# Kernel tuning notes

Measured on AMD Instinct MI355X. Metric: run time of the kernel, lower is better.

## Reference

```python
import jax, jax.numpy as jnp
import numpy as np

N_CODES = 1024
CODE_DIM = 256
B, T = 64, 1024


def setup_inputs() -> dict:
    key = jax.random.key(0)
    k1, k2 = jax.random.split(key)
    inputs = jax.random.normal(k1, (B, CODE_DIM, T), dtype=jnp.float32)
    embed = jax.random.normal(k2, (N_CODES, CODE_DIM), dtype=jnp.float32)
    return {"inputs": inputs, "embed": embed, "training": 0}


def reference(inputs, embed, training):
    # inputs: [B, D, T] -> [B, T, D]
    x = jnp.transpose(inputs, (0, 2, 1))
    Bsz, Tlen, D = x.shape
    flat = x.reshape(-1, D)  # [N, D], N = B*T
    distances = (
        jnp.sum(flat * flat, axis=1, keepdims=True)
        - 2.0 * jnp.matmul(flat, embed.T)
        + jnp.sum(embed * embed, axis=1)
    )  # [N, n_codes]
    encoding_indices = jnp.argmin(distances, axis=1)  # [N]
    # gather instead of one-hot matmul (same math)
    quantized = embed[encoding_indices].reshape(x.shape)  # [B, T, D]

    sg = jax.lax.stop_gradient
    codebook_loss = jnp.mean((sg(quantized) - x) ** 2)
    cmt_loss = jnp.mean((quantized - sg(x)) ** 2)
    loss = codebook_loss + cmt_loss * 0.2

    # straight-through estimator
    quantized_st = x + sg(quantized - x)
    quantized_out = jnp.transpose(quantized_st, (0, 2, 1))  # [B, D, T]

    # avg one-hot probabilities via bincount-style scatter-add
    n = flat.shape[0]
    counts = jnp.zeros((N_CODES,), dtype=flat.dtype).at[encoding_indices].add(1.0)
    avg_probs = counts / n
    perplexity = jnp.exp(-jnp.sum(avg_probs * jnp.log(avg_probs + 1e-10)))

    encoding_indices_out = encoding_indices.reshape(Bsz, -1, 1)
    return (quantized_out, loss, cmt_loss, encoding_indices_out, perplexity)
```

## Files before the change

### kernel.cpp

```cpp
#include <hip/hip_runtime.h>

#define B_ 64
#define D_ 256
#define T_ 1024
#define NC_ 1024
#define DT_ (D_ * T_)
#define NPTS_ (B_ * T_)

#define QSZ_   16777216
#define LOSS_OFF 16777216
#define CMT_OFF  16777217
#define IDX_OFF  16777218
#define PERP_OFF 16842754

typedef _Float16 half8 __attribute__((ext_vector_type(8)));
typedef float f32x4 __attribute__((ext_vector_type(4)));

#define XROW_ 264
#define XLO_OFF_ (64 * XROW_)

__global__ void prep_embed(const float* __restrict__ embed,
                           _Float16* __restrict__ ehi,
                           _Float16* __restrict__ elo,
                           float* __restrict__ normf) {
  int g = blockIdx.x;
  int tid = threadIdx.x;
  int w = tid >> 6, l = tid & 63;

#pragma unroll
  for (int ii = 0; ii < 2; ++ii) {
    int kc = w * 2 + ii;
    int code = g * 16 + (l & 15);
    int k0 = kc * 32 + (l >> 4) * 8;
    const float* src = embed + (size_t)code * D_ + k0;
    half8 hh, ll;
#pragma unroll
    for (int j = 0; j < 8; ++j) {
      float v = src[j];
      _Float16 h = (_Float16)v;
      _Float16 lo = (_Float16)(v - (float)h);
      hh[j] = h;
      ll[j] = lo;
    }
    size_t off = ((size_t)(g * 8 + kc) * 64 + l) * 8;
    *(half8*)(ehi + off) = hh;
    *(half8*)(elo + off) = ll;
  }

  int code = g * 16 + (tid >> 4);
  int ks = (tid & 15) * 16;
  const float* src = embed + (size_t)code * D_ + ks;
  double s = 0.0;
#pragma unroll
  for (int j = 0; j < 16; ++j) {
    double v = src[j];
    s += v * v;
  }
#pragma unroll
  for (int m = 1; m < 16; m <<= 1) s += __shfl_xor(s, m, 64);
  if ((tid & 15) == 0) normf[code] = (float)s;
}

__global__ __launch_bounds__(256, 2) void argmin_kernel(
    const float* __restrict__ inputs, const _Float16* __restrict__ ehi,
    const _Float16* __restrict__ elo, const float* __restrict__ normf,
    float* __restrict__ idx_out, int* __restrict__ counts,
    double* __restrict__ mse_acc) {
  __shared__ _Float16 xs[2 * 64 * XROW_];
  __shared__ float normf_lds[1024];
  __shared__ double part[256];
  __shared__ double xn2s[64];

  float* candv = (float*)part;
  int* candi = (int*)&part[128];

  int tid = threadIdx.x;
  int blk = blockIdx.x;
  int b = blk >> 4, t0 = (blk & 15) * 64;
  size_t base = (size_t)b * DT_ + t0;

  {
    int t = tid & 63, dgrp = tid >> 6;
    const float* src = inputs + base + t;
    double s = 0.0;
#pragma unroll 4
    for (int i = 0; i < 32; ++i) {
      int d = dgrp * 64 + i * 2;
      float v0 = src[(size_t)d * T_];
      float v1 = src[(size_t)(d + 1) * T_];
      s += (double)v0 * v0 + (double)v1 * v1;
      _Float16 h0 = (_Float16)v0, h1 = (_Float16)v1;
      _Float16 e0 = (_Float16)(v0 - (float)h0);
      _Float16 e1 = (_Float16)(v1 - (float)h1);
      union {
        _Float16 h[2];
        unsigned u;
      } ph, pl;
      ph.h[0] = h0; ph.h[1] = h1;
      pl.h[0] = e0; pl.h[1] = e1;
      *(unsigned*)&xs[t * XROW_ + d] = ph.u;
      *(unsigned*)&xs[XLO_OFF_ + t * XROW_ + d] = pl.u;
    }
    part[tid] = s;
    ((float4*)normf_lds)[tid] = ((const float4*)normf)[tid];
  }
  __syncthreads();
  if (tid < 64)
    xn2s[tid] = part[tid] + part[64 + tid] + part[128 + tid] + part[192 + tid];
  __syncthreads();

  int w = tid >> 6, l = tid & 63;
  int lrow = l & 15;
  int lk = (l >> 4) * 8;

  float bestv[4][4];
  int besti[4][4];
#pragma unroll
  for (int m = 0; m < 4; ++m)
#pragma unroll
    for (int r = 0; r < 4; ++r) {
      bestv[m][r] = 1e30f;
      besti[m][r] = 0;
    }

#pragma unroll 1
  for (int ng = 0; ng < 4; ++ng) {
    f32x4 acc[4][4];
#pragma unroll
    for (int m = 0; m < 4; ++m)
#pragma unroll
      for (int n = 0; n < 4; ++n) acc[m][n] = (f32x4){0.f, 0.f, 0.f, 0.f};

#pragma unroll 2
    for (int kc = 0; kc < 8; ++kc) {
      half8 bh[4], bl[4];
#pragma unroll
      for (int n = 0; n < 4; ++n) {
        int g = ng * 16 + w * 4 + n;
        size_t off = ((size_t)(g * 8 + kc) * 64 + l) * 8;
        bh[n] = *(const half8*)(ehi + off);
        bl[n] = *(const half8*)(elo + off);
      }
      half8 ah[4], al[4];
#pragma unroll
      for (int m = 0; m < 4; ++m) {
        const _Float16* p = &xs[(m * 16 + lrow) * XROW_ + kc * 32 + lk];
        ah[m] = *(const half8*)p;
        al[m] = *(const half8*)(p + XLO_OFF_);
      }
#pragma unroll
      for (int m = 0; m < 4; ++m)
#pragma unroll
        for (int n = 0; n < 4; ++n) {
          acc[m][n] =
              __builtin_amdgcn_mfma_f32_16x16x32_f16(ah[m], bh[n], acc[m][n], 0, 0, 0);
          acc[m][n] =
              __builtin_amdgcn_mfma_f32_16x16x32_f16(al[m], bh[n], acc[m][n], 0, 0, 0);
          acc[m][n] =
              __builtin_amdgcn_mfma_f32_16x16x32_f16(ah[m], bl[n], acc[m][n], 0, 0, 0);
        }
    }

#pragma unroll
    for (int n = 0; n < 4; ++n) {
      int c = ng * 256 + w * 64 + n * 16 + lrow;
      float nf = normf_lds[c];
#pragma unroll
      for (int m = 0; m < 4; ++m)
#pragma unroll
        for (int r = 0; r < 4; ++r) {
          float df = fmaf(-2.0f, acc[m][n][r], nf);
          if (df < bestv[m][r]) {
            bestv[m][r] = df;
            besti[m][r] = c;
          }
        }
    }
  }

#pragma unroll
  for (int msk = 1; msk < 16; msk <<= 1) {
#pragma unroll
    for (int m = 0; m < 4; ++m)
#pragma unroll
      for (int r = 0; r < 4; ++r) {
        float ov = __shfl_xor(bestv[m][r], msk, 64);
        int oi = __shfl_xor(besti[m][r], msk, 64);
        if (ov < bestv[m][r] || (ov == bestv[m][r] && oi < besti[m][r])) {
          bestv[m][r] = ov;
          besti[m][r] = oi;
        }
      }
  }
  if (lrow == 0) {
    int q = l >> 4;
#pragma unroll
    for (int m = 0; m < 4; ++m)
#pragma unroll
      for (int r = 0; r < 4; ++r) {
        candv[w * 64 + m * 16 + q * 4 + r] = bestv[m][r];
        candi[w * 64 + m * 16 + q * 4 + r] = besti[m][r];
      }
  }
  __syncthreads();

  if (tid < 64) {
    float bv = candv[tid];
    int bi = candi[tid];
#pragma unroll
    for (int w2 = 1; w2 < 4; ++w2) {
      float ov = candv[w2 * 64 + tid];
      int oi = candi[w2 * 64 + tid];
      if (ov < bv || (ov == bv && oi < bi)) {
        bv = ov;
        bi = oi;
      }
    }
    int p = blk * 64 + tid;
    idx_out[p] = (float)bi;
    atomicAdd(&counts[bi], 1);
    double s = xn2s[tid] + (double)bv;
    for (int msk = 32; msk; msk >>= 1) s += __shfl_down(s, msk, 64);
    if (tid == 0) atomicAdd(mse_acc, s);
  }
}

__global__ __launch_bounds__(256) void quantize_kernel(
    const float* __restrict__ embed, const float* __restrict__ idx_f,
    float* __restrict__ qout) {
  __shared__ float qs[64 * 257];
  __shared__ int lidx[64];

  int tid = threadIdx.x;
  int bx = blockIdx.x;
  int b = bx >> 4;
  int t0 = (bx & 15) * 64;

  if (tid < 64) lidx[tid] = (int)idx_f[b * T_ + t0 + tid];
  __syncthreads();

#pragma unroll 4
  for (int p = 0; p < 64; ++p) {
    qs[p * 257 + tid] = embed[(size_t)lidx[p] * D_ + tid];
  }
  __syncthreads();

  size_t base = (size_t)b * DT_ + t0;
#pragma unroll 4
  for (int i = 0; i < 64; ++i) {
    int d = i * 4 + (tid >> 6);
    int p = tid & 63;
    qout[base + (size_t)d * T_ + p] = qs[p * 257 + d];
  }
}

__global__ void finalize_kernel(const int* __restrict__ counts,
                                const double* __restrict__ mse_acc,
                                float* __restrict__ out) {
  int tid = threadIdx.x;
  double p = (double)counts[tid] / (double)NPTS_;
  double s = p * log(p + 1e-10);
  for (int m = 32; m; m >>= 1) s += __shfl_down(s, m, 64);
  __shared__ double red[16];
  if ((tid & 63) == 0) red[tid >> 6] = s;
  __syncthreads();
  if (tid == 0) {
    double tot = 0.0;
    for (int i = 0; i < 16; ++i) tot += red[i];
    double mse = *mse_acc / (double)QSZ_;
    out[LOSS_OFF] = (float)(mse * 1.2);
    out[CMT_OFF] = (float)mse;
    out[PERP_OFF] = (float)exp(-tot);
  }
}

extern "C" void kernel_launch(void* const* d_in, const int* in_sizes, int n_in,
                              void* d_out, int out_size, void* d_ws,
                              size_t ws_size, hipStream_t stream) {
  const float* inputs = (const float*)d_in[0];
  const float* embed = (const float*)d_in[1];
  float* out = (float*)d_out;

  char* ws = (char*)d_ws;
  _Float16* ehi = (_Float16*)ws;
  _Float16* elo = (_Float16*)(ws + 524288);
  float* normf = (float*)(ws + 1048576);
  int* counts = (int*)(ws + 1048576 + 4096);
  double* mse = (double*)(ws + 1048576 + 8192);

  hipMemsetAsync(ws + 1048576 + 4096, 0, 4096 + 8, stream);

  prep_embed<<<64, 256, 0, stream>>>(embed, ehi, elo, normf);
  argmin_kernel<<<1024, 256, 0, stream>>>(inputs, ehi, elo, normf,
                                          out + IDX_OFF, counts, mse);
  quantize_kernel<<<1024, 256, 0, stream>>>(embed, out + IDX_OFF, out);
  finalize_kernel<<<1, 1024, 0, stream>>>(counts, mse, out);
}
```

Baseline: 151.2 us.

## Software-pipeline argmin MFMA loop with double-buffered operands and narrower code tiles

Restructures the argmin GEMM loop so each wave handles 2 code tiles per group across 8 groups instead of 4 tiles across 4 groups. Loads for the next k-chunk of global B and LDS A fragments are issued into a second register buffer while MFMAs run on the current one. The aim is to hide global and LDS latency behind matrix math and cut accumulator register pressure. In exchange, the X fragments are now reloaded from LDS twice as often, and the last step prefetches group 0 again, which is wasted work.

Measured after the change: 339.4 us. 124% more time.

```diff
diff --git a/kernel.cpp b/kernel.cpp
--- a/kernel.cpp
+++ b/kernel.cpp
@@ -59,6 +59,46 @@
 #pragma unroll
   for (int m = 1; m < 16; m <<= 1) s += __shfl_xor(s, m, 64);
   if ((tid & 15) == 0) normf[code] = (float)s;
+}
+
+__device__ __forceinline__ void loadB2(half8 (&BH)[2], half8 (&BL)[2],
+                                       const _Float16* __restrict__ ehi,
+                                       const _Float16* __restrict__ elo,
+                                       int w, int l, int ng, int kc) {
+#pragma unroll
+  for (int n = 0; n < 2; ++n) {
+    int g = ng * 8 + w * 2 + n;
+    size_t off = ((size_t)(g * 8 + kc) * 64 + l) * 8;
+    BH[n] = *(const half8*)(ehi + off);
+    BL[n] = *(const half8*)(elo + off);
+  }
+}
+
+__device__ __forceinline__ void loadA(half8 (&AH)[4], half8 (&AL)[4],
+                                      const _Float16* xs, int lrow, int lk,
+                                      int kc) {
+#pragma unroll
+  for (int m = 0; m < 4; ++m) {
+    const _Float16* p = &xs[(m * 16 + lrow) * XROW_ + kc * 32 + lk];
+    AH[m] = *(const half8*)p;
+    AL[m] = *(const half8*)(p + XLO_OFF_);
+  }
+}
+
+__device__ __forceinline__ void mfma24(f32x4 (&acc)[4][2], half8 (&AH)[4],
+                                       half8 (&AL)[4], half8 (&BH)[2],
+                                       half8 (&BL)[2]) {
+#pragma unroll
+  for (int m = 0; m < 4; ++m)
+#pragma unroll
+    for (int n = 0; n < 2; ++n) {
+      acc[m][n] =
+          __builtin_amdgcn_mfma_f32_16x16x32_f16(AH[m], BH[n], acc[m][n], 0, 0, 0);
+      acc[m][n] =
+          __builtin_amdgcn_mfma_f32_16x16x32_f16(AL[m], BH[n], acc[m][n], 0, 0, 0);
+      acc[m][n] =
+          __builtin_amdgcn_mfma_f32_16x16x32_f16(AH[m], BL[n], acc[m][n], 0, 0, 0);
+    }
 }
 
 __global__ __launch_bounds__(256, 2) void argmin_kernel(
@@ -72,7 +112,7 @@
   __shared__ double xn2s[64];
 
   float* candv = (float*)part;
-  int* candi = (int*)&part[128];
+  int* candi = (int*)(part + 128);
 
   int tid = threadIdx.x;
   int blk = blockIdx.x;
@@ -123,47 +163,42 @@
       besti[m][r] = 0;
     }
 
+  half8 ahA[4], alA[4], ahB[4], alB[4];
+  half8 bhA[2], blA[2], bhB[2], blB[2];
+  loadB2(bhA, blA, ehi, elo, w, l, 0, 0);
+  loadA(ahA, alA, xs, lrow, lk, 0);
+
+#define STEP_TO_B(NGB, KCB, KCA)                       \
+  loadB2(bhB, blB, ehi, elo, w, l, NGB, KCB);          \
+  loadA(ahB, alB, xs, lrow, lk, KCA);                  \
+  mfma24(acc, ahA, alA, bhA, blA);
+
+#define STEP_TO_A(NGB, KCB, KCA)                       \
+  loadB2(bhA, blA, ehi, elo, w, l, NGB, KCB);          \
+  loadA(ahA, alA, xs, lrow, lk, KCA);                  \
+  mfma24(acc, ahB, alB, bhB, blB);
+
 #pragma unroll 1
-  for (int ng = 0; ng < 4; ++ng) {
-    f32x4 acc[4][4];
+  for (int ng = 0; ng < 8; ++ng) {
+    f32x4 acc[4][2];
 #pragma unroll
     for (int m = 0; m < 4; ++m)
 #pragma unroll
-      for (int n = 0; n < 4; ++n) acc[m][n] = (f32x4){0.f, 0.f, 0.f, 0.f};
-
-#pragma unroll 2
-    for (int kc = 0; kc < 8; ++kc) {
-      half8 bh[4], bl[4];
-#pragma unroll
-      for (int n = 0; n < 4; ++n) {
-        int g = ng * 16 + w * 4 + n;
-        size_t off = ((size_t)(g * 8 + kc) * 64 + l) * 8;
-        bh[n] = *(const half8*)(ehi + off);
-        bl[n] = *(const half8*)(elo + off);
-      }
-      half8 ah[4], al[4];
-#pragma unroll
-      for (int m = 0; m < 4; ++m) {
-        const _Float16* p = &xs[(m * 16 + lrow) * XROW_ + kc * 32 + lk];
-        ah[m] = *(const half8*)p;
-        al[m] = *(const half8*)(p + XLO_OFF_);
-      }
-#pragma unroll
-      for (int m = 0; m < 4; ++m)
-#pragma unroll
-        for (int n = 0; n < 4; ++n) {
-          acc[m][n] =
-              __builtin_amdgcn_mfma_f32_16x16x32_f16(ah[m], bh[n], acc[m][n], 0, 0, 0);
-          acc[m][n] =
-              __builtin_amdgcn_mfma_f32_16x16x32_f16(al[m], bh[n], acc[m][n], 0, 0, 0);
-          acc[m][n] =
-              __builtin_amdgcn_mfma_f32_16x16x32_f16(ah[m], bl[n], acc[m][n], 0, 0, 0);
-        }
-    }
-
-#pragma unroll
-    for (int n = 0; n < 4; ++n) {
-      int c = ng * 256 + w * 64 + n * 16 + lrow;
+      for (int n = 0; n < 2; ++n) acc[m][n] = (f32x4){0.f, 0.f, 0.f, 0.f};
+
+    int ngn = (ng + 1) & 7;
+    STEP_TO_B(ng, 1, 1)
+    STEP_TO_A(ng, 2, 2)
+    STEP_TO_B(ng, 3, 3)
+    STEP_TO_A(ng, 4, 4)
+    STEP_TO_B(ng, 5, 5)
+    STEP_TO_A(ng, 6, 6)
+    STEP_TO_B(ng, 7, 7)
+    STEP_TO_A(ngn, 0, 0)
+
+#pragma unroll
+    for (int n = 0; n < 2; ++n) {
+      int c = (ng * 8 + w * 2 + n) * 16 + lrow;
       float nf = normf_lds[c];
 #pragma unroll
       for (int m = 0; m < 4; ++m)
@@ -177,6 +212,8 @@
         }
     }
   }
+#undef STEP_TO_B
+#undef STEP_TO_A
 
 #pragma unroll
   for (int msk = 1; msk < 16; msk <<= 1) {
```

## Keep input tile in registers and stream codebook through double-buffered LDS

Applied to the files above, without the earlier changes.

Each wave now holds its own 16 points' split-f16 A fragments in registers for the whole K range. The hi/lo codebook is streamed in 16-code chunks into double-buffered LDS using global_load_lds, so all four waves share each chunk instead of each wave reading its own codes from global memory. This removes the per-wave global B traffic and the cross-wave argmin reduction, and raises occupancy to 3 blocks per CU. In exchange it needs a barrier every one of 64 iterations and does only one MFMA chain per iteration, which may leave latency exposed. It also relies on every lane of a predicated group reaching the atomics and shuffles correctly.

Result: slower. 176.8 us (+16.9%).

```diff
diff --git a/kernel.cpp b/kernel.cpp
--- a/kernel.cpp
+++ b/kernel.cpp
@@ -16,9 +16,6 @@
 typedef _Float16 half8 __attribute__((ext_vector_type(8)));
 typedef float f32x4 __attribute__((ext_vector_type(4)));
 
-#define XROW_ 264
-#define XLO_OFF_ (64 * XROW_)
-
 __global__ void prep_embed(const float* __restrict__ embed,
                            _Float16* __restrict__ ehi,
                            _Float16* __restrict__ elo,
@@ -61,167 +58,135 @@
   if ((tid & 15) == 0) normf[code] = (float)s;
 }
 
-__global__ __launch_bounds__(256, 2) void argmin_kernel(
+__device__ __forceinline__ void gld_lds16(const _Float16* gsrc_lane,
+                                          _Float16* lds_base) {
+  __builtin_amdgcn_global_load_lds(
+      (const __attribute__((address_space(1))) void*)gsrc_lane,
+      (__attribute__((address_space(3))) void*)lds_base, 16, 0, 0);
+}
+
+__global__ __launch_bounds__(256, 3) void argmin_kernel(
     const float* __restrict__ inputs, const _Float16* __restrict__ ehi,
     const _Float16* __restrict__ elo, const float* __restrict__ normf,
     float* __restrict__ idx_out, int* __restrict__ counts,
     double* __restrict__ mse_acc) {
-  __shared__ _Float16 xs[2 * 64 * XROW_];
+  __shared__ _Float16 ldsB[2][8192];
   __shared__ float normf_lds[1024];
-  __shared__ double part[256];
-  __shared__ double xn2s[64];
-
-  float* candv = (float*)part;
-  int* candi = (int*)&part[128];
+  __shared__ double xn2w[64];
 
   int tid = threadIdx.x;
   int blk = blockIdx.x;
   int b = blk >> 4, t0 = (blk & 15) * 64;
-  size_t base = (size_t)b * DT_ + t0;
-
+  int w = tid >> 6, l = tid & 63;
+
+  half8 ah[8], al[8];
+  double xn2p = 0.0;
   {
-    int t = tid & 63, dgrp = tid >> 6;
-    const float* src = inputs + base + t;
+    const float* xsrc = inputs + (size_t)b * DT_ + t0 + w * 16 + (l & 15);
+    int kbase = (l >> 4) * 8;
+#pragma unroll
+    for (int kc = 0; kc < 8; ++kc) {
+      half8 hh, ll;
+#pragma unroll
+      for (int j = 0; j < 8; ++j) {
+        float v = xsrc[(size_t)(kc * 32 + kbase + j) * T_];
+        xn2p += (double)v * v;
+        _Float16 h = (_Float16)v;
+        _Float16 lo = (_Float16)(v - (float)h);
+        hh[j] = h;
+        ll[j] = lo;
+      }
+      ah[kc] = hh;
+      al[kc] = ll;
+    }
+  }
+  xn2p += __shfl_xor(xn2p, 16, 64);
+  xn2p += __shfl_xor(xn2p, 32, 64);
+  if (l < 16) xn2w[w * 16 + l] = xn2p;
+
+  ((float4*)normf_lds)[tid] = ((const float4*)normf)[tid];
+#pragma unroll
+  for (int i = 0; i < 2; ++i) {
+    int kc = w * 2 + i;
+    size_t off = ((size_t)kc * 64 + l) * 8;
+    gld_lds16(ehi + off, &ldsB[0][kc * 512]);
+    gld_lds16(elo + off, &ldsB[0][4096 + kc * 512]);
+  }
+  __syncthreads();
+
+  float bestv[4];
+  int besti[4];
+#pragma unroll
+  for (int j = 0; j < 4; ++j) {
+    bestv[j] = 1e30f;
+    besti[j] = 0;
+  }
+
+#pragma unroll 1
+  for (int t = 0; t < 64; ++t) {
+    int cur = t & 1, nxt = cur ^ 1;
+    if (t < 63) {
+#pragma unroll
+      for (int i = 0; i < 2; ++i) {
+        int kc = w * 2 + i;
+        size_t off = ((size_t)((t + 1) * 8 + kc) * 64 + l) * 8;
+        gld_lds16(ehi + off, &ldsB[nxt][kc * 512]);
+        gld_lds16(elo + off, &ldsB[nxt][4096 + kc * 512]);
+      }
+    }
+
+    f32x4 acc = (f32x4){0.f, 0.f, 0.f, 0.f};
+#pragma unroll
+    for (int kc = 0; kc < 8; ++kc) {
+      half8 bh = *(const half8*)&ldsB[cur][(kc * 64 + l) * 8];
+      half8 bl = *(const half8*)&ldsB[cur][4096 + (kc * 64 + l) * 8];
+      acc = __builtin_amdgcn_mfma_f32_16x16x32_f16(ah[kc], bh, acc, 0, 0, 0);
+      acc = __builtin_amdgcn_mfma_f32_16x16x32_f16(al[kc], bh, acc, 0, 0, 0);
+      acc = __builtin_amdgcn_mfma_f32_16x16x32_f16(ah[kc], bl, acc, 0, 0, 0);
+    }
+
+    {
+      int c = t * 16 + (l & 15);
+      float nf = normf_lds[c];
+#pragma unroll
+      for (int j = 0; j < 4; ++j) {
+        float df = fmaf(-2.0f, acc[j], nf);
+        if (df < bestv[j]) {
+          bestv[j] = df;
+          besti[j] = c;
+        }
+      }
+    }
+    __syncthreads();
+  }
+
+#pragma unroll
+  for (int msk = 1; msk < 16; msk <<= 1) {
+#pragma unroll
+    for (int j = 0; j < 4; ++j) {
+      float ov = __shfl_xor(bestv[j], msk, 64);
+      int oi = __shfl_xor(besti[j], msk, 64);
+      if (ov < bestv[j] || (ov == bestv[j] && oi < besti[j])) {
+        bestv[j] = ov;
+        besti[j] = oi;
+      }
+    }
+  }
+
+  if ((l & 15) == 0) {
+    float4 iw;
     double s = 0.0;
-#pragma unroll 4
-    for (int i = 0; i < 32; ++i) {
-      int d = dgrp * 64 + i * 2;
-      float v0 = src[(size_t)d * T_];
-      float v1 = src[(size_t)(d + 1) * T_];
-      s += (double)v0 * v0 + (double)v1 * v1;
-      _Float16 h0 = (_Float16)v0, h1 = (_Float16)v1;
-      _Float16 e0 = (_Float16)(v0 - (float)h0);
-      _Float16 e1 = (_Float16)(v1 - (float)h1);
-      union {
-        _Float16 h[2];
-        unsigned u;
-      } ph, pl;
-      ph.h[0] = h0; ph.h[1] = h1;
-      pl.h[0] = e0; pl.h[1] = e1;
-      *(unsigned*)&xs[t * XROW_ + d] = ph.u;
-      *(unsigned*)&xs[XLO_OFF_ + t * XROW_ + d] = pl.u;
-    }
-    part[tid] = s;
-    ((float4*)normf_lds)[tid] = ((const float4*)normf)[tid];
-  }
-  __syncthreads();
-  if (tid < 64)
-    xn2s[tid] = part[tid] + part[64 + tid] + part[128 + tid] + part[192 + tid];
-  __syncthreads();
-
-  int w = tid >> 6, l = tid & 63;
-  int lrow = l & 15;
-  int lk = (l >> 4) * 8;
-
-  float bestv[4][4];
-  int besti[4][4];
-#pragma unroll
-  for (int m = 0; m < 4; ++m)
-#pragma unroll
-    for (int r = 0; r < 4; ++r) {
-      bestv[m][r] = 1e30f;
-      besti[m][r] = 0;
-    }
-
-#pragma unroll 1
-  for (int ng = 0; ng < 4; ++ng) {
-    f32x4 acc[4][4];
-#pragma unroll
-    for (int m = 0; m < 4; ++m)
-#pragma unroll
-      for (int n = 0; n < 4; ++n) acc[m][n] = (f32x4){0.f, 0.f, 0.f, 0.f};
-
-#pragma unroll 2
-    for (int kc = 0; kc < 8; ++kc) {
-      half8 bh[4], bl[4];
-#pragma unroll
-      for (int n = 0; n < 4; ++n) {
-        int g = ng * 16 + w * 4 + n;
-        size_t off = ((size_t)(g * 8 + kc) * 64 + l) * 8;
-        bh[n] = *(const half8*)(ehi + off);
-        bl[n] = *(const half8*)(elo + off);
-      }
-      half8 ah[4], al[4];
-#pragma unroll
-      for (int m = 0; m < 4; ++m) {
-        const _Float16* p = &xs[(m * 16 + lrow) * XROW_ + kc * 32 + lk];
-        ah[m] = *(const half8*)p;
-        al[m] = *(const half8*)(p + XLO_OFF_);
-      }
-#pragma unroll
-      for (int m = 0; m < 4; ++m)
-#pragma unroll
-        for (int n = 0; n < 4; ++n) {
-          acc[m][n] =
-              __builtin_amdgcn_mfma_f32_16x16x32_f16(ah[m], bh[n], acc[m][n], 0, 0, 0);
-          acc[m][n] =
-              __builtin_amdgcn_mfma_f32_16x16x32_f16(al[m], bh[n], acc[m][n], 0, 0, 0);
-          acc[m][n] =
-              __builtin_amdgcn_mfma_f32_16x16x32_f16(ah[m], bl[n], acc[m][n], 0, 0, 0);
-        }
-    }
-
-#pragma unroll
-    for (int n = 0; n < 4; ++n) {
-      int c = ng * 256 + w * 64 + n * 16 + lrow;
-      float nf = normf_lds[c];
-#pragma unroll
-      for (int m = 0; m < 4; ++m)
-#pragma unroll
-        for (int r = 0; r < 4; ++r) {
-          float df = fmaf(-2.0f, acc[m][n][r], nf);
-          if (df < bestv[m][r]) {
-            bestv[m][r] = df;
-            besti[m][r] = c;
-          }
-        }
-    }
-  }
-
-#pragma unroll
-  for (int msk = 1; msk < 16; msk <<= 1) {
-#pragma unroll
-    for (int m = 0; m < 4; ++m)
-#pragma unroll
-      for (int r = 0; r < 4; ++r) {
-        float ov = __shfl_xor(bestv[m][r], msk, 64);
-        int oi = __shfl_xor(besti[m][r], msk, 64);
-        if (ov < bestv[m][r] || (ov == bestv[m][r] && oi < besti[m][r])) {
-          bestv[m][r] = ov;
-          besti[m][r] = oi;
-        }
-      }
-  }
-  if (lrow == 0) {
-    int q = l >> 4;
-#pragma unroll
-    for (int m = 0; m < 4; ++m)
-#pragma unroll
-      for (int r = 0; r < 4; ++r) {
-        candv[w * 64 + m * 16 + q * 4 + r] = bestv[m][r];
-        candi[w * 64 + m * 16 + q * 4 + r] = besti[m][r];
-      }
-  }
-  __syncthreads();
-
-  if (tid < 64) {
-    float bv = candv[tid];
-    int bi = candi[tid];
-#pragma unroll
-    for (int w2 = 1; w2 < 4; ++w2) {
-      float ov = candv[w2 * 64 + tid];
-      int oi = candi[w2 * 64 + tid];
-      if (ov < bv || (ov == bv && oi < bi)) {
-        bv = ov;
-        bi = oi;
-      }
-    }
-    int p = blk * 64 + tid;
-    idx_out[p] = (float)bi;
-    atomicAdd(&counts[bi], 1);
-    double s = xn2s[tid] + (double)bv;
-    for (int msk = 32; msk; msk >>= 1) s += __shfl_down(s, msk, 64);
-    if (tid == 0) atomicAdd(mse_acc, s);
+#pragma unroll
+    for (int j = 0; j < 4; ++j) {
+      int p = (l >> 4) * 4 + j;
+      iw[j == 0 ? 0 : (j == 1 ? 1 : (j == 2 ? 2 : 3))] = (float)besti[j];
+      atomicAdd(&counts[besti[j]], 1);
+      s += xn2w[w * 16 + p] + (double)bestv[j];
+    }
+    *(float4*)&idx_out[blk * 64 + w * 16 + (l >> 4) * 4] = iw;
+    s += __shfl_xor(s, 16, 64);
+    s += __shfl_xor(s, 32, 64);
+    if (l == 0) atomicAdd(mse_acc, s);
   }
 }
 
```
